# Kernel tuning notes

Hardware: AMD Instinct MI355X
Metric: run time of the kernel (lower is better)

The kernel has to match this reference:

```python
import jax, jax.numpy as jnp
import numpy as np

D_MODEL = 1024
NUM_HEADS = 16
SEQ_LEN = 2048
WINDOW_SIZES = (5, 10, 20, 40)


def _avg_gaussian_mask(seq_len, dtype=jnp.float32):
    # mask[i,j] = exp(-(i-j)^2/(2 w^2)) if j <= i else 0; averaged over 4 windows.
    i = jnp.arange(seq_len, dtype=dtype)[:, None]
    j = jnp.arange(seq_len, dtype=dtype)[None, :]
    d2 = (i - j) ** 2
    lower = (j <= i)
    masks = [jnp.where(lower, jnp.exp(-d2 / (2.0 * w * w)), 0.0) for w in WINDOW_SIZES]
    return sum(masks) / len(WINDOW_SIZES)  # [S, S]


def setup_inputs() -> dict:
    key = jax.random.key(0)
    ks = jax.random.split(key, 11)
    B, S, D = 2, SEQ_LEN, D_MODEL
    std = 1.0 / np.sqrt(D)
    inp = {
        "Q": jax.random.normal(ks[0], (B, S, D), jnp.float32),
        "K": jax.random.normal(ks[1], (B, S, D), jnp.float32),
        "V": jax.random.normal(ks[2], (B, S, D), jnp.float32),
        "Wq": jax.random.uniform(ks[3], (D, D), jnp.float32, -std, std),
        "bq": jax.random.uniform(ks[4], (D,), jnp.float32, -std, std),
        "Wk": jax.random.uniform(ks[5], (D, D), jnp.float32, -std, std),
        "bk": jax.random.uniform(ks[6], (D,), jnp.float32, -std, std),
        "Wv": jax.random.uniform(ks[7], (D, D), jnp.float32, -std, std),
        "bv": jax.random.uniform(ks[8], (D,), jnp.float32, -std, std),
        "Wo": jax.random.uniform(ks[9], (D, D), jnp.float32, -std, std),
        "bo": jax.random.uniform(ks[10], (D,), jnp.float32, -std, std),
    }
    return inp


def reference(Q, K, V, Wq, bq, Wk, bk, Wv, bv, Wo, bo):
    B, S, D = Q.shape
    H, dk = NUM_HEADS, D // NUM_HEADS

    def proj(x, W, b):
        # torch Linear: x @ W^T + b, then split heads -> [B, H, S, dk]
        y = x @ W.T + b
        return y.reshape(B, S, H, dk).transpose(0, 2, 1, 3)

    q = proj(Q, Wq, bq)
    k = proj(K, Wk, bk)
    v = proj(V, Wv, bv)

    # mean over mask dim of (scores + mask_m) == scores + mean(mask)
    avg_mask = _avg_gaussian_mask(S, q.dtype)  # [S, S]
    scores = jnp.einsum('bhqd,bhkd->bhqk', q, k) / jnp.sqrt(jnp.asarray(dk, q.dtype))
    scores = scores + avg_mask  # broadcast over [B, H]
    probs = jax.nn.softmax(scores, axis=-1)
    out = jnp.einsum('bhqk,bhkd->bhqd', probs, v)
    out = out.transpose(0, 2, 1, 3).reshape(B, S, D)
    return out @ Wo.T + bo
```

## Files before the change

### kernel.cpp

```cpp
#include <hip/hip_runtime.h>
#include <hip/hip_bf16.h>


#define S_LEN 2048
#define D_MODEL 1024
#define NHEADS 16
#define DK 64
#define BATCH 2
#define M_ROWS (BATCH * S_LEN)
#define LOG2E 1.4426950408889634f

typedef float f32x4 __attribute__((ext_vector_type(4)));
typedef short s16x8 __attribute__((ext_vector_type(8)));
typedef unsigned short u16x8 __attribute__((ext_vector_type(8)));
typedef unsigned u32x4 __attribute__((ext_vector_type(4)));

__device__ __forceinline__ unsigned short f2bf(float f) {
    unsigned u = __builtin_bit_cast(unsigned, f);
    u = (u + 0x7FFFu + ((u >> 16) & 1u)) >> 16;
    return (unsigned short)u;
}

__device__ __forceinline__ float fast_exp2(float x) {
    float r;
    asm("v_exp_f32 %0, %1" : "=v"(r) : "v"(x));
    return r;
}

__device__ __forceinline__ unsigned cvt_pk_bf16(float a, float b) {
    unsigned r;
    asm("v_cvt_pk_bf16_f32 %0, %1, %2" : "=v"(r) : "v"(a), "v"(b));
    return r;
}

#define GLD16(gptr, lptr)                                                     \
    __builtin_amdgcn_global_load_lds(                                         \
        (const __attribute__((address_space(1))) void*)(gptr),                \
        (__attribute__((address_space(3))) void*)(lptr), 16, 0, 0)

__global__ __launch_bounds__(256) void convert_kernel(
    const float* __restrict__ Q, const float* __restrict__ K,
    const float* __restrict__ V,
    const float* __restrict__ Wq, const float* __restrict__ Wk,
    const float* __restrict__ Wv, const float* __restrict__ Wo,
    unsigned short* __restrict__ Qb, unsigned short* __restrict__ Kb,
    unsigned short* __restrict__ Vb,
    unsigned short* __restrict__ Wqb, unsigned short* __restrict__ Wkb,
    unsigned short* __restrict__ Wvb, unsigned short* __restrict__ Wob,
    float* __restrict__ mtab)
{
    const int XN = M_ROWS * D_MODEL / 8;
    const int WN = D_MODEL * D_MODEL / 8;
    const int TOT = 3 * XN + 4 * WN;
    int i = blockIdx.x * 256 + threadIdx.x;
    if (i >= TOT) {
        int d = i - TOT;
        if (d < S_LEN) {
            float d2 = (float)d * (float)d;
            mtab[d] = LOG2E * 0.25f * (__expf(-d2 * (1.0f / 50.0f)) +
                                       __expf(-d2 * (1.0f / 200.0f)) +
                                       __expf(-d2 * (1.0f / 800.0f)) +
                                       __expf(-d2 * (1.0f / 3200.0f)));
        }
        return;
    }
    const float* src;
    unsigned short* dst;
    int off;
    if (i < 3 * XN) {
        if (i < XN)          { src = Q; dst = Qb; off = i; }
        else if (i < 2 * XN) { src = K; dst = Kb; off = i - XN; }
        else                 { src = V; dst = Vb; off = i - 2 * XN; }
    } else {
        int j = i - 3 * XN;
        if (j < WN)          { src = Wq; dst = Wqb; off = j; }
        else if (j < 2 * WN) { src = Wk; dst = Wkb; off = j - WN; }
        else if (j < 3 * WN) { src = Wv; dst = Wvb; off = j - 2 * WN; }
        else                 { src = Wo; dst = Wob; off = j - 3 * WN; }
    }
    f32x4 v0 = *(const f32x4*)(src + (size_t)off * 8);
    f32x4 v1 = *(const f32x4*)(src + (size_t)off * 8 + 4);
    s16x8 o;
#pragma unroll
    for (int j = 0; j < 4; ++j) {
        o[j]     = (short)f2bf(v0[j]);
        o[j + 4] = (short)f2bf(v1[j]);
    }
    *(s16x8*)(dst + (size_t)off * 8) = o;
}

__device__ __forceinline__ void gemm_core_128(
    const unsigned short* __restrict__ A, const unsigned short* __restrict__ B,
    unsigned short* As, unsigned short* Bs,
    int m0, int n0, int K, int tid, f32x4 acc[4][4])
{
    const int wid  = tid >> 6;
    const int lane = tid & 63;
    const int g    = lane >> 4;
    const int c    = lane & 15;
    const int wm   = wid >> 1;
    const int wn   = wid & 1;

    const int srow   = tid >> 3;
    const int schunk = tid & 7;

    for (int kt = 0; kt < K / 64; ++kt) {
        const int k0 = kt * 64;
        __syncthreads();
#pragma unroll
        for (int r = 0; r < 4; ++r) {
            const int row = r * 32 + srow;
            GLD16(A + (size_t)(m0 + row) * K + k0 + schunk * 8,
                  &As[(r * 256 + wid * 64) * 8]);
        }
#pragma unroll
        for (int r = 0; r < 4; ++r) {
            const int row = r * 32 + srow;
            GLD16(B + (size_t)(n0 + row) * K + k0 + schunk * 8,
                  &Bs[(r * 256 + wid * 64) * 8]);
        }
        __syncthreads();

        s16x8 a[2][4];
#pragma unroll
        for (int ks = 0; ks < 2; ++ks)
#pragma unroll
            for (int mf = 0; mf < 4; ++mf)
                a[ks][mf] = *(const s16x8*)
                    &As[(wm * 64 + mf * 16 + c) * 64 + ks * 32 + g * 8];
#pragma unroll
        for (int ks = 0; ks < 2; ++ks) {
#pragma unroll
            for (int nf = 0; nf < 4; ++nf) {
                s16x8 b = *(const s16x8*)
                    &Bs[(wn * 64 + nf * 16 + c) * 64 + ks * 32 + g * 8];
#pragma unroll
                for (int mf = 0; mf < 4; ++mf)
                    acc[mf][nf] = __builtin_amdgcn_mfma_f32_16x16x32_bf16(
                        a[ks][mf], b, acc[mf][nf], 0, 0, 0);
            }
        }
    }
}

__global__ __launch_bounds__(256) void proj_gemm(
    const unsigned short* __restrict__ Qx, const unsigned short* __restrict__ Kx,
    const unsigned short* __restrict__ Vx,
    const unsigned short* __restrict__ Wq, const unsigned short* __restrict__ Wk,
    const unsigned short* __restrict__ Wv,
    const float* __restrict__ bq, const float* __restrict__ bk,
    const float* __restrict__ bv,
    unsigned short* __restrict__ qo, unsigned short* __restrict__ ko,
    unsigned short* __restrict__ vo)
{
    const int z = blockIdx.z;
    const unsigned short* X = (z == 0) ? Qx : (z == 1) ? Kx : Vx;
    const unsigned short* W = (z == 0) ? Wq : (z == 1) ? Wk : Wv;
    const float* bias       = (z == 0) ? bq : (z == 1) ? bk : bv;
    unsigned short* out     = (z == 0) ? qo : (z == 1) ? ko : vo;
    const float scale = (z == 0) ? (0.125f * LOG2E) : 1.0f;

    __shared__ unsigned short As[128 * 64];
    __shared__ unsigned short Bs[128 * 64];

    const int tid = threadIdx.x;
    const int flat = blockIdx.y * 32 + blockIdx.x;
    const int sw   = (flat & 7) * 32 + (flat >> 3);
    const int m0   = (sw & 31) * 128;
    const int n0   = (sw >> 5) * 128;

    f32x4 acc[4][4];
#pragma unroll
    for (int i = 0; i < 4; ++i)
#pragma unroll
        for (int j = 0; j < 4; ++j) acc[i][j] = (f32x4){0.f, 0.f, 0.f, 0.f};

    gemm_core_128(X, W, As, Bs, m0, n0, D_MODEL, tid, acc);

    const int lane = tid & 63;
    const int g    = lane >> 4;
    const int c    = lane & 15;
    const int wm   = (tid >> 6) >> 1;
    const int wn   = (tid >> 6) & 1;

#pragma unroll
    for (int mf = 0; mf < 4; ++mf) {
#pragma unroll
        for (int nf = 0; nf < 4; ++nf) {
            const int o = n0 + wn * 64 + nf * 16 + c;
            const float bv_ = bias[o];
            const int h  = o >> 6;
            const int dd = o & 63;
#pragma unroll
            for (int r = 0; r < 4; ++r) {
                const int m = m0 + wm * 64 + mf * 16 + g * 4 + r;
                const int b = m >> 11;
                const int s = m & (S_LEN - 1);
                const float val = (acc[mf][nf][r] + bv_) * scale;
                out[(((size_t)(b * NHEADS + h)) * S_LEN + s) * DK + dd] = f2bf(val);
            }
        }
    }
}

__global__ __launch_bounds__(256) void out_gemm(
    const unsigned short* __restrict__ A,
    const unsigned short* __restrict__ W,
    const float* __restrict__ bias,
    float* __restrict__ out)
{
    __shared__ unsigned short As[128 * 64];
    __shared__ unsigned short Bs[128 * 64];

    const int tid = threadIdx.x;
    const int flat = blockIdx.y * 32 + blockIdx.x;
    const int sw   = (flat & 7) * 32 + (flat >> 3);
    const int m0   = (sw & 31) * 128;
    const int n0   = (sw >> 5) * 128;

    f32x4 acc[4][4];
#pragma unroll
    for (int i = 0; i < 4; ++i)
#pragma unroll
        for (int j = 0; j < 4; ++j) acc[i][j] = (f32x4){0.f, 0.f, 0.f, 0.f};

    gemm_core_128(A, W, As, Bs, m0, n0, D_MODEL, tid, acc);

    const int lane = tid & 63;
    const int g    = lane >> 4;
    const int c    = lane & 15;
    const int wm   = (tid >> 6) >> 1;
    const int wn   = (tid >> 6) & 1;

#pragma unroll
    for (int mf = 0; mf < 4; ++mf) {
#pragma unroll
        for (int nf = 0; nf < 4; ++nf) {
            const int o = n0 + wn * 64 + nf * 16 + c;
            const float bv_ = bias[o];
#pragma unroll
            for (int r = 0; r < 4; ++r) {
                const int m = m0 + wm * 64 + mf * 16 + g * 4 + r;
                out[(size_t)m * D_MODEL + o] = acc[mf][nf][r] + bv_;
            }
        }
    }
}

#define SWZ(row)  ((((row) & 7) ^ ((((row) >> 3) & 1) << 2)) << 4)
#define VSWZ(row) ((((row) >> 1) & 7) << 4)

__global__ __launch_bounds__(256) void attn_kernel(
    const unsigned short* __restrict__ qh,
    const unsigned short* __restrict__ kh,
    const unsigned short* __restrict__ vh,
    const float* __restrict__ mask_tab,
    unsigned short* __restrict__ attn_out)
{
    __shared__ float mtab[S_LEN];
    __shared__ unsigned short Kt[2][64 * 64];
    __shared__ unsigned short Vt[2][64 * 64];

    const int tid  = threadIdx.x;
    const int wid  = tid >> 6;
    const int lane = tid & 63;
    const int g    = lane >> 4;
    const int c    = lane & 15;

    const int flat = blockIdx.y * 16 + blockIdx.x;
    const int sw   = (flat & 7) * 64 + (flat >> 3);
    const int bh   = sw >> 4;
    const int bx   = sw & 15;
    const int b    = bh >> 4;
    const int h    = bh & 15;
    const int q0w  = bx * 128 + wid * 32;

    *(f32x4*)&mtab[tid * 8]     = *(const f32x4*)&mask_tab[tid * 8];
    *(f32x4*)&mtab[tid * 8 + 4] = *(const f32x4*)&mask_tab[tid * 8 + 4];

    const size_t head_off = (size_t)bh * S_LEN * DK;
    const unsigned short* qp = qh + head_off;
    const unsigned short* kp = kh + head_off;
    const unsigned short* vp = vh + head_off;

    s16x8 aq[2][2];
#pragma unroll
    for (int qf = 0; qf < 2; ++qf) {
        const unsigned short* qrow = qp + (size_t)(q0w + qf * 16 + c) * DK;
        aq[qf][0] = *(const s16x8*)(qrow + g * 8);
        aq[qf][1] = *(const s16x8*)(qrow + 32 + g * 8);
    }

    f32x4 acc_o[2][4];
#pragma unroll
    for (int qf = 0; qf < 2; ++qf)
#pragma unroll
        for (int nf = 0; nf < 4; ++nf) acc_o[qf][nf] = (f32x4){0.f, 0.f, 0.f, 0.f};
    f32x4 lsum[2];
    lsum[0] = (f32x4){0.f, 0.f, 0.f, 0.f};
    lsum[1] = (f32x4){0.f, 0.f, 0.f, 0.f};

    int krow_nf[4];
#pragma unroll
    for (int nf = 0; nf < 4; ++nf)
        krow_nf[nf] = ((c >> 2) << 3) + ((nf & 1) << 2) + (c & 3) + ((nf >> 1) << 5);

    const int srowK  = tid >> 2;
    const int kchunk = (tid & 3) * 16;
    const int vd0    = (tid & 31) * 2;
    const int vk8    = (tid >> 5) * 8;

    s16x8 kr0, kr1;
    unsigned vr[8];

    kr0 = *(const s16x8*)&kp[(size_t)srowK * DK + kchunk];
    kr1 = *(const s16x8*)&kp[(size_t)srowK * DK + kchunk + 8];
#pragma unroll
    for (int i = 0; i < 8; ++i)
        vr[i] = *(const unsigned*)&vp[(size_t)(vk8 + i) * DK + vd0];
    {
        char* kb = (char*)Kt[0] + srowK * 128;
        *(s16x8*)(kb + ((kchunk * 2) ^ SWZ(srowK)))      = kr0;
        *(s16x8*)(kb + ((kchunk * 2 + 16) ^ SWZ(srowK))) = kr1;
        u16x8 lo, hi8;
#pragma unroll
        for (int i = 0; i < 8; ++i) {
            lo[i]  = (unsigned short)vr[i];
            hi8[i] = (unsigned short)(vr[i] >> 16);
        }
        *(u16x8*)((char*)Vt[0] + vd0 * 128 + ((vk8 * 2) ^ VSWZ(vd0)))           = lo;
        *(u16x8*)((char*)Vt[0] + (vd0 + 1) * 128 + ((vk8 * 2) ^ VSWZ(vd0 + 1))) = hi8;
    }
    kr0 = *(const s16x8*)&kp[(size_t)(64 + srowK) * DK + kchunk];
    kr1 = *(const s16x8*)&kp[(size_t)(64 + srowK) * DK + kchunk + 8];
#pragma unroll
    for (int i = 0; i < 8; ++i)
        vr[i] = *(const unsigned*)&vp[(size_t)(64 + vk8 + i) * DK + vd0];
    __syncthreads();

    const int NT = S_LEN / 64;
    for (int kt = 0; kt < NT; ++kt) {
        const int k0 = kt * 64;
        const int cur = kt & 1;
        const unsigned short* Kc = Kt[cur];
        const unsigned short* Vc = Vt[cur];

        if (kt + 1 < NT) {
            char* kb = (char*)Kt[cur ^ 1] + srowK * 128;
            *(s16x8*)(kb + ((kchunk * 2) ^ SWZ(srowK)))      = kr0;
            *(s16x8*)(kb + ((kchunk * 2 + 16) ^ SWZ(srowK))) = kr1;
            u16x8 lo, hi8;
#pragma unroll
            for (int i = 0; i < 8; ++i) {
                lo[i]  = (unsigned short)vr[i];
                hi8[i] = (unsigned short)(vr[i] >> 16);
            }
            *(u16x8*)((char*)Vt[cur ^ 1] + vd0 * 128 +
                      ((vk8 * 2) ^ VSWZ(vd0))) = lo;
            *(u16x8*)((char*)Vt[cur ^ 1] + (vd0 + 1) * 128 +
                      ((vk8 * 2) ^ VSWZ(vd0 + 1))) = hi8;
            if (kt + 2 < NT) {
                const int k2 = k0 + 128;
                kr0 = *(const s16x8*)&kp[(size_t)(k2 + srowK) * DK + kchunk];
                kr1 = *(const s16x8*)&kp[(size_t)(k2 + srowK) * DK + kchunk + 8];
#pragma unroll
                for (int i = 0; i < 8; ++i)
                    vr[i] = *(const unsigned*)&vp[(size_t)(k2 + vk8 + i) * DK + vd0];
            }
        }

        f32x4 st[2][4];
        __builtin_amdgcn_s_setprio(1);
#pragma unroll
        for (int nf = 0; nf < 4; ++nf) {
            st[0][nf] = (f32x4){0.f, 0.f, 0.f, 0.f};
            st[1][nf] = (f32x4){0.f, 0.f, 0.f, 0.f};
            const int row = krow_nf[nf];
#pragma unroll
            for (int f = 0; f < 2; ++f) {
                s16x8 kf = *(const s16x8*)((const char*)Kc + row * 128 +
                                           ((f * 64 + g * 16) ^ SWZ(row)));
                st[0][nf] = __builtin_amdgcn_mfma_f32_16x16x32_bf16(
                    kf, aq[0][f], st[0][nf], 0, 0, 0);
                st[1][nf] = __builtin_amdgcn_mfma_f32_16x16x32_bf16(
                    kf, aq[1][f], st[1][nf], 0, 0, 0);
            }
        }
        __builtin_amdgcn_s_setprio(0);

        const int diff = q0w - k0;
        if (diff >= -31 && diff <= 510) {
#pragma unroll
            for (int qf = 0; qf < 2; ++qf) {
                const int dbase = q0w + qf * 16 + c - k0 - g * 8;
#pragma unroll
                for (int nf = 0; nf < 4; ++nf) {
                    const int koff = ((nf & 1) << 2) + ((nf >> 1) << 5);
#pragma unroll
                    for (int r = 0; r < 4; ++r) {
                        const int d = dbase - koff - r;
                        if (d >= 0) st[qf][nf][r] += mtab[d];
                    }
                }
            }
        }

        u32x4 pa[2][2];
#pragma unroll
        for (int qf = 0; qf < 2; ++qf) {
#pragma unroll
            for (int nf = 0; nf < 4; ++nf)
#pragma unroll
                for (int r = 0; r < 4; ++r)
                    st[qf][nf][r] = fast_exp2(st[qf][nf][r]);
            lsum[qf] += (st[qf][0] + st[qf][1]) + (st[qf][2] + st[qf][3]);
#pragma unroll
            for (int f = 0; f < 2; ++f) {
                pa[qf][f][0] = cvt_pk_bf16(st[qf][2 * f][0],     st[qf][2 * f][1]);
                pa[qf][f][1] = cvt_pk_bf16(st[qf][2 * f][2],     st[qf][2 * f][3]);
                pa[qf][f][2] = cvt_pk_bf16(st[qf][2 * f + 1][0], st[qf][2 * f + 1][1]);
                pa[qf][f][3] = cvt_pk_bf16(st[qf][2 * f + 1][2], st[qf][2 * f + 1][3]);
            }
        }

        __builtin_amdgcn_s_setprio(1);
#pragma unroll
        for (int f = 0; f < 2; ++f) {
            s16x8 pa0 = __builtin_bit_cast(s16x8, pa[0][f]);
            s16x8 pa1 = __builtin_bit_cast(s16x8, pa[1][f]);
#pragma unroll
            for (int nf = 0; nf < 4; ++nf) {
                const int row = nf * 16 + c;
                s16x8 vb = *(const s16x8*)((const char*)Vc + row * 128 +
                                           ((f * 64 + g * 16) ^ VSWZ(row)));
                acc_o[0][nf] = __builtin_amdgcn_mfma_f32_16x16x32_bf16(
                    pa0, vb, acc_o[0][nf], 0, 0, 0);
                acc_o[1][nf] = __builtin_amdgcn_mfma_f32_16x16x32_bf16(
                    pa1, vb, acc_o[1][nf], 0, 0, 0);
            }
        }
        __builtin_amdgcn_s_setprio(0);

        __syncthreads();
    }

#pragma unroll
    for (int qf = 0; qf < 2; ++qf) {
        float l = (lsum[qf][0] + lsum[qf][1]) + (lsum[qf][2] + lsum[qf][3]);
        l += __shfl_xor(l, 16);
        l += __shfl_xor(l, 32);
        f32x4 linv;
#pragma unroll
        for (int r = 0; r < 4; ++r) linv[r] = 1.0f / __shfl(l, g * 4 + r);
#pragma unroll
        for (int nf = 0; nf < 4; ++nf) {
#pragma unroll
            for (int r = 0; r < 4; ++r) {
                const int i_glob = q0w + qf * 16 + g * 4 + r;
                const int d = nf * 16 + c;
                attn_out[((size_t)(b * S_LEN + i_glob)) * D_MODEL + h * DK + d] =
                    f2bf(acc_o[qf][nf][r] * linv[r]);
            }
        }
    }
}

extern "C" void kernel_launch(void* const* d_in, const int* in_sizes, int n_in,
                              void* d_out, int out_size, void* d_ws, size_t ws_size,
                              hipStream_t stream) {
    const float* Q  = (const float*)d_in[0];
    const float* K  = (const float*)d_in[1];
    const float* V  = (const float*)d_in[2];
    const float* Wq = (const float*)d_in[3];
    const float* bq = (const float*)d_in[4];
    const float* Wk = (const float*)d_in[5];
    const float* bk = (const float*)d_in[6];
    const float* Wv = (const float*)d_in[7];
    const float* bv = (const float*)d_in[8];
    const float* Wo = (const float*)d_in[9];
    const float* bo = (const float*)d_in[10];
    float* out = (float*)d_out;

    const size_t XE = (size_t)M_ROWS * D_MODEL;
    const size_t WE = (size_t)D_MODEL * D_MODEL;
    unsigned short* qh  = (unsigned short*)d_ws;
    unsigned short* kh  = qh + XE;
    unsigned short* vh  = kh + XE;
    unsigned short* ah  = vh + XE;
    unsigned short* Qb  = ah + XE;
    unsigned short* Kb  = Qb + XE;
    unsigned short* Vb  = Kb + XE;
    unsigned short* Wqb = Vb + XE;
    unsigned short* Wkb = Wqb + WE;
    unsigned short* Wvb = Wkb + WE;
    unsigned short* Wob = Wvb + WE;
    float* mtab = (float*)(Wob + WE);

    convert_kernel<<<dim3((3 * XE / 8 + 4 * WE / 8) / 256 + 8), 256, 0, stream>>>(
        Q, K, V, Wq, Wk, Wv, Wo, Qb, Kb, Vb, Wqb, Wkb, Wvb, Wob, mtab);
    proj_gemm<<<dim3(32, 8, 3), 256, 0, stream>>>(
        Qb, Kb, Vb, Wqb, Wkb, Wvb, bq, bk, bv, qh, kh, vh);
    attn_kernel<<<dim3(16, 32), 256, 0, stream>>>(
        qh, kh, vh, mtab, ah);
    out_gemm<<<dim3(32, 8), 256, 0, stream>>>(
        ah, Wob, bo, out);
}
```

Before: 147.7 us.

## Split attention key range across wave pairs and merge partial results in LDS

```diff
diff --git a/kernel.cpp b/kernel.cpp
--- a/kernel.cpp
+++ b/kernel.cpp
@@ -12,7 +12,7 @@
 
 typedef float f32x4 __attribute__((ext_vector_type(4)));
 typedef short s16x8 __attribute__((ext_vector_type(8)));
-typedef unsigned short u16x8 __attribute__((ext_vector_type(8)));
+typedef unsigned short u16x4 __attribute__((ext_vector_type(4)));
 typedef unsigned u32x4 __attribute__((ext_vector_type(4)));
 
 __device__ __forceinline__ unsigned short f2bf(float f) {
@@ -250,7 +250,7 @@
 #define SWZ(row)  ((((row) & 7) ^ ((((row) >> 3) & 1) << 2)) << 4)
 #define VSWZ(row) ((((row) >> 1) & 7) << 4)
 
-__global__ __launch_bounds__(256) void attn_kernel(
+__global__ __launch_bounds__(512) void attn_kernel(
     const unsigned short* __restrict__ qh,
     const unsigned short* __restrict__ kh,
     const unsigned short* __restrict__ vh,
@@ -260,12 +260,15 @@
     __shared__ float mtab[S_LEN];
     __shared__ unsigned short Kt[2][64 * 64];
     __shared__ unsigned short Vt[2][64 * 64];
+    __shared__ float lmerge[512];
 
     const int tid  = threadIdx.x;
     const int wid  = tid >> 6;
     const int lane = tid & 63;
     const int g    = lane >> 4;
     const int c    = lane & 15;
+    const int qg   = wid >> 1;
+    const int par  = wid & 1;
 
     const int flat = blockIdx.y * 16 + blockIdx.x;
     const int sw   = (flat & 7) * 64 + (flat >> 3);
@@ -273,10 +276,9 @@
     const int bx   = sw & 15;
     const int b    = bh >> 4;
     const int h    = bh & 15;
-    const int q0w  = bx * 128 + wid * 32;
-
-    *(f32x4*)&mtab[tid * 8]     = *(const f32x4*)&mask_tab[tid * 8];
-    *(f32x4*)&mtab[tid * 8 + 4] = *(const f32x4*)&mask_tab[tid * 8 + 4];
+    const int q0w  = bx * 128 + qg * 32;
+
+    *(f32x4*)&mtab[tid * 4] = *(const f32x4*)&mask_tab[tid * 4];
 
     const size_t head_off = (size_t)bh * S_LEN * DK;
     const unsigned short* qp = qh + head_off;
@@ -305,69 +307,49 @@
     for (int nf = 0; nf < 4; ++nf)
         krow_nf[nf] = ((c >> 2) << 3) + ((nf & 1) << 2) + (c & 3) + ((nf >> 1) << 5);
 
-    const int srowK  = tid >> 2;
-    const int kchunk = (tid & 3) * 16;
-    const int vd0    = (tid & 31) * 2;
-    const int vk8    = (tid >> 5) * 8;
-
-    s16x8 kr0, kr1;
-    unsigned vr[8];
-
-    kr0 = *(const s16x8*)&kp[(size_t)srowK * DK + kchunk];
-    kr1 = *(const s16x8*)&kp[(size_t)srowK * DK + kchunk + 8];
-#pragma unroll
-    for (int i = 0; i < 8; ++i)
-        vr[i] = *(const unsigned*)&vp[(size_t)(vk8 + i) * DK + vd0];
-    {
-        char* kb = (char*)Kt[0] + srowK * 128;
-        *(s16x8*)(kb + ((kchunk * 2) ^ SWZ(srowK)))      = kr0;
-        *(s16x8*)(kb + ((kchunk * 2 + 16) ^ SWZ(srowK))) = kr1;
-        u16x8 lo, hi8;
-#pragma unroll
-        for (int i = 0; i < 8; ++i) {
-            lo[i]  = (unsigned short)vr[i];
-            hi8[i] = (unsigned short)(vr[i] >> 16);
-        }
-        *(u16x8*)((char*)Vt[0] + vd0 * 128 + ((vk8 * 2) ^ VSWZ(vd0)))           = lo;
-        *(u16x8*)((char*)Vt[0] + (vd0 + 1) * 128 + ((vk8 * 2) ^ VSWZ(vd0 + 1))) = hi8;
-    }
-    kr0 = *(const s16x8*)&kp[(size_t)(64 + srowK) * DK + kchunk];
-    kr1 = *(const s16x8*)&kp[(size_t)(64 + srowK) * DK + kchunk + 8];
-#pragma unroll
-    for (int i = 0; i < 8; ++i)
-        vr[i] = *(const unsigned*)&vp[(size_t)(64 + vk8 + i) * DK + vd0];
+    const int srowK = tid >> 3;
+    const int soffE = (tid & 7) * 8;
+    const int vd0   = (tid & 31) * 2;
+    const int vkq   = (tid >> 5) * 4;
+
+    s16x8 krA, krB;
+    unsigned vrA[4], vrB[4];
+
+    krA = *(const s16x8*)&kp[(size_t)srowK * DK + soffE];
+    krB = *(const s16x8*)&kp[(size_t)(64 + srowK) * DK + soffE];
+#pragma unroll
+    for (int i = 0; i < 4; ++i) {
+        vrA[i] = *(const unsigned*)&vp[(size_t)(vkq + i) * DK + vd0];
+        vrB[i] = *(const unsigned*)&vp[(size_t)(64 + vkq + i) * DK + vd0];
+    }
+#pragma unroll
+    for (int t = 0; t < 2; ++t) {
+        s16x8 kr = t ? krB : krA;
+        *(s16x8*)((char*)Kt[t] + srowK * 128 + ((soffE * 2) ^ SWZ(srowK))) = kr;
+        u16x4 lo4, hi4;
+#pragma unroll
+        for (int i = 0; i < 4; ++i) {
+            unsigned v = t ? vrB[i] : vrA[i];
+            lo4[i] = (unsigned short)v;
+            hi4[i] = (unsigned short)(v >> 16);
+        }
+        *(u16x4*)((char*)Vt[t] + vd0 * 128 + ((vkq * 2) ^ VSWZ(vd0)))           = lo4;
+        *(u16x4*)((char*)Vt[t] + (vd0 + 1) * 128 + ((vkq * 2) ^ VSWZ(vd0 + 1))) = hi4;
+    }
+    krA = *(const s16x8*)&kp[(size_t)(128 + srowK) * DK + soffE];
+    krB = *(const s16x8*)&kp[(size_t)(192 + srowK) * DK + soffE];
+#pragma unroll
+    for (int i = 0; i < 4; ++i) {
+        vrA[i] = *(const unsigned*)&vp[(size_t)(128 + vkq + i) * DK + vd0];
+        vrB[i] = *(const unsigned*)&vp[(size_t)(192 + vkq + i) * DK + vd0];
+    }
     __syncthreads();
 
-    const int NT = S_LEN / 64;
-    for (int kt = 0; kt < NT; ++kt) {
-        const int k0 = kt * 64;
-        const int cur = kt & 1;
-        const unsigned short* Kc = Kt[cur];
-        const unsigned short* Vc = Vt[cur];
-
-        if (kt + 1 < NT) {
-            char* kb = (char*)Kt[cur ^ 1] + srowK * 128;
-            *(s16x8*)(kb + ((kchunk * 2) ^ SWZ(srowK)))      = kr0;
-            *(s16x8*)(kb + ((kchunk * 2 + 16) ^ SWZ(srowK))) = kr1;
-            u16x8 lo, hi8;
-#pragma unroll
-            for (int i = 0; i < 8; ++i) {
-                lo[i]  = (unsigned short)vr[i];
-                hi8[i] = (unsigned short)(vr[i] >> 16);
-            }
-            *(u16x8*)((char*)Vt[cur ^ 1] + vd0 * 128 +
-                      ((vk8 * 2) ^ VSWZ(vd0))) = lo;
-            *(u16x8*)((char*)Vt[cur ^ 1] + (vd0 + 1) * 128 +
-                      ((vk8 * 2) ^ VSWZ(vd0 + 1))) = hi8;
-            if (kt + 2 < NT) {
-                const int k2 = k0 + 128;
-                kr0 = *(const s16x8*)&kp[(size_t)(k2 + srowK) * DK + kchunk];
-                kr1 = *(const s16x8*)&kp[(size_t)(k2 + srowK) * DK + kchunk + 8];
-#pragma unroll
-                for (int i = 0; i < 8; ++i)
-                    vr[i] = *(const unsigned*)&vp[(size_t)(k2 + vk8 + i) * DK + vd0];
-            }
-        }
+    const int NP = S_LEN / 128;
+    for (int p = 0; p < NP; ++p) {
+        const int k0 = (p * 2 + par) * 64;
+        const unsigned short* Kc = Kt[par];
+        const unsigned short* Vc = Vt[par];
 
         f32x4 st[2][4];
         __builtin_amdgcn_s_setprio(1);
@@ -442,24 +424,86 @@
         __builtin_amdgcn_s_setprio(0);
 
         __syncthreads();
-    }
-
+
+        if (p + 1 < NP) {
+#pragma unroll
+            for (int t = 0; t < 2; ++t) {
+                s16x8 kr = t ? krB : krA;
+                *(s16x8*)((char*)Kt[t] + srowK * 128 +
+                          ((soffE * 2) ^ SWZ(srowK))) = kr;
+                u16x4 lo4, hi4;
+#pragma unroll
+                for (int i = 0; i < 4; ++i) {
+                    unsigned v = t ? vrB[i] : vrA[i];
+                    lo4[i] = (unsigned short)v;
+                    hi4[i] = (unsigned short)(v >> 16);
+                }
+                *(u16x4*)((char*)Vt[t] + vd0 * 128 +
+                          ((vkq * 2) ^ VSWZ(vd0))) = lo4;
+                *(u16x4*)((char*)Vt[t] + (vd0 + 1) * 128 +
+                          ((vkq * 2) ^ VSWZ(vd0 + 1))) = hi4;
+            }
+            if (p + 2 < NP) {
+                const int kb = (p + 2) * 128;
+                krA = *(const s16x8*)&kp[(size_t)(kb + srowK) * DK + soffE];
+                krB = *(const s16x8*)&kp[(size_t)(kb + 64 + srowK) * DK + soffE];
+#pragma unroll
+                for (int i = 0; i < 4; ++i) {
+                    vrA[i] = *(const unsigned*)&vp[(size_t)(kb + vkq + i) * DK + vd0];
+                    vrB[i] = *(const unsigned*)&vp[(size_t)(kb + 64 + vkq + i) * DK + vd0];
+                }
+            }
+            __syncthreads();
+        }
+    }
+
+    float lq[2];
 #pragma unroll
     for (int qf = 0; qf < 2; ++qf) {
         float l = (lsum[qf][0] + lsum[qf][1]) + (lsum[qf][2] + lsum[qf][3]);
         l += __shfl_xor(l, 16);
         l += __shfl_xor(l, 32);
-        f32x4 linv;
-#pragma unroll
-        for (int r = 0; r < 4; ++r) linv[r] = 1.0f / __shfl(l, g * 4 + r);
-#pragma unroll
-        for (int nf = 0; nf < 4; ++nf) {
-#pragma unroll
-            for (int r = 0; r < 4; ++r) {
-                const int i_glob = q0w + qf * 16 + g * 4 + r;
-                const int d = nf * 16 + c;
-                attn_out[((size_t)(b * S_LEN + i_glob)) * D_MODEL + h * DK + d] =
-                    f2bf(acc_o[qf][nf][r] * linv[r]);
+        lq[qf] = l;
+    }
+    float* pool = (qg < 2) ? ((float*)Kt + qg * 2048)
+                           : ((float*)Vt + (qg - 2) * 2048);
+    if (par) {
+#pragma unroll
+        for (int qf = 0; qf < 2; ++qf)
+#pragma unroll
+            for (int nf = 0; nf < 4; ++nf)
+#pragma unroll
+                for (int r = 0; r < 4; ++r)
+                    pool[(qf * 16 + nf * 4 + r) * 64 + lane] = acc_o[qf][nf][r];
+        lmerge[(qg * 2 + 0) * 64 + lane] = lq[0];
+        lmerge[(qg * 2 + 1) * 64 + lane] = lq[1];
+    }
+    __syncthreads();
+    if (!par) {
+#pragma unroll
+        for (int qf = 0; qf < 2; ++qf)
+#pragma unroll
+            for (int nf = 0; nf < 4; ++nf)
+#pragma unroll
+                for (int r = 0; r < 4; ++r)
+                    acc_o[qf][nf][r] += pool[(qf * 16 + nf * 4 + r) * 64 + lane];
+        lq[0] += lmerge[(qg * 2 + 0) * 64 + lane];
+        lq[1] += lmerge[(qg * 2 + 1) * 64 + lane];
+
+#pragma unroll
+        for (int qf = 0; qf < 2; ++qf) {
+            f32x4 linv;
+#pragma unroll
+            for (int r = 0; r < 4; ++r) linv[r] = 1.0f / __shfl(lq[qf], g * 4 + r);
+#pragma unroll
+            for (int nf = 0; nf < 4; ++nf) {
+#pragma unroll
+                for (int r = 0; r < 4; ++r) {
+                    const int i_glob = q0w + qf * 16 + g * 4 + r;
+                    const int d = nf * 16 + c;
+                    attn_out[((size_t)(b * S_LEN + i_glob)) * D_MODEL + h * DK + d] =
+                        f2bf(acc_o[qf][nf][r] * linv[r]);
+                }
             }
         }
     }
@@ -500,7 +544,7 @@
         Q, K, V, Wq, Wk, Wv, Wo, Qb, Kb, Vb, Wqb, Wkb, Wvb, Wob, mtab);
     proj_gemm<<<dim3(32, 8, 3), 256, 0, stream>>>(
         Qb, Kb, Vb, Wqb, Wkb, Wvb, bq, bk, bv, qh, kh, vh);
-    attn_kernel<<<dim3(16, 32), 256, 0, stream>>>(
+    attn_kernel<<<dim3(16, 32), 512, 0, stream>>>(
         qh, kh, vh, mtab, ah);
     out_gemm<<<dim3(32, 8), 256, 0, stream>>>(
         ah, Wob, bo, out);
```

After: 140.5 us. 4.8% less time.
